# Optimization experiments

Measured on AMD Instinct MI355X. Metric: run time of the kernel, lower is better.

## Reference

```python
import jax, jax.numpy as jnp
import numpy as np

B, SEQ, DIM = 2, 2048, 1024
HEADS, HEAD_DIM = 16, 64
HIDDEN = 2816
EPS = 1e-5
LN_EPS = 1e-5


def rmsnorm(x, w, eps=EPS):
    return x * jax.lax.rsqrt(jnp.mean(x * x, axis=-1, keepdims=True) + eps) * w


def layernorm(x, w, b, eps=LN_EPS):
    mu = jnp.mean(x, axis=-1, keepdims=True)
    var = jnp.mean((x - mu) ** 2, axis=-1, keepdims=True)
    return (x - mu) * jax.lax.rsqrt(var + eps) * w + b


def modulate(x, shift, scale):
    # x: [B,S,D], shift/scale: [B,D]
    return x * (1.0 + scale[:, None, :]) + shift[:, None, :]


def apply_rope(t, cos, sin):
    # t: [B,S,H,D]; cos/sin: [S, D/2] -> complex multiply on (even,odd) pairs
    t = t.reshape(*t.shape[:-1], HEAD_DIM // 2, 2)
    t0, t1 = t[..., 0], t[..., 1]
    c = cos[None, :, None, :]
    s = sin[None, :, None, :]
    o0 = t0 * c - t1 * s
    o1 = t0 * s + t1 * c
    return jnp.stack([o0, o1], axis=-1).reshape(*t.shape[:-2], HEAD_DIM)


def setup_inputs() -> dict:
    key = jax.random.key(0)
    ks = jax.random.split(key, 12)
    def w(k, shape, s=0.02):
        return jax.random.normal(k, shape, dtype=jnp.float32) * s
    x = jax.random.normal(ks[0], (B, SEQ, DIM), dtype=jnp.float32)
    adaln_input = jax.random.normal(ks[1], (B, DIM), dtype=jnp.float32)
    pos = jnp.arange(SEQ, dtype=jnp.float32)
    inv_freq = 1.0 / (10000.0 ** (jnp.arange(0, HEAD_DIM, 2, dtype=jnp.float32) / HEAD_DIM))
    ang = pos[:, None] * inv_freq[None, :]  # [S, D/2]
    return dict(
        x=x, adaln_input=adaln_input,
        freqs_cos=jnp.cos(ang), freqs_sin=jnp.sin(ang),
        wq=w(ks[2], (DIM, DIM)), wk=w(ks[3], (DIM, DIM)),
        wv=w(ks[4], (DIM, DIM)), wo=w(ks[5], (DIM, DIM)),
        q_norm_w=jnp.ones(DIM, jnp.float32), q_norm_b=jnp.zeros(DIM, jnp.float32),
        k_norm_w=jnp.ones(DIM, jnp.float32), k_norm_b=jnp.zeros(DIM, jnp.float32),
        attn_norm_w=jnp.ones(DIM, jnp.float32), ffn_norm_w=jnp.ones(DIM, jnp.float32),
        ada_w=w(ks[6], (DIM, 6 * DIM)), ada_b=jnp.zeros(6 * DIM, jnp.float32),
        w1=w(ks[7], (DIM, HIDDEN)), w2=w(ks[8], (HIDDEN, DIM)), w3=w(ks[9], (DIM, HIDDEN)),
    )


def reference(x, adaln_input, freqs_cos, freqs_sin, wq, wk, wv, wo,
              q_norm_w, q_norm_b, k_norm_w, k_norm_b,
              attn_norm_w, ffn_norm_w, ada_w, ada_b, w1, w2, w3):
    # adaLN modulation: SiLU -> Linear -> 6 chunks of [B, DIM]
    m = jax.nn.silu(adaln_input) @ ada_w + ada_b
    shift_msa, scale_msa, gate_msa, shift_mlp, scale_mlp, gate_mlp = jnp.split(m, 6, axis=1)

    # --- attention branch ---
    h = modulate(rmsnorm(x, attn_norm_w), shift_msa, scale_msa)
    xq = layernorm(h @ wq, q_norm_w, q_norm_b)
    xk = layernorm(h @ wk, k_norm_w, k_norm_b)
    xv = h @ wv
    xq = xq.reshape(B, SEQ, HEADS, HEAD_DIM)
    xk = xk.reshape(B, SEQ, HEADS, HEAD_DIM)
    xv = xv.reshape(B, SEQ, HEADS, HEAD_DIM)
    xq = apply_rope(xq, freqs_cos, freqs_sin)
    xk = apply_rope(xk, freqs_cos, freqs_sin)
    scale = 1.0 / jnp.sqrt(jnp.float32(HEAD_DIM))
    scores = jnp.einsum('bshd,bthd->bhst', xq, xk) * scale  # [B,H,S,S]
    probs = jax.nn.softmax(scores, axis=-1)
    attn = jnp.einsum('bhst,bthd->bshd', probs, xv).reshape(B, SEQ, DIM)
    attn = attn @ wo
    x = x + gate_msa[:, None, :] * attn

    # --- MLP branch (SwiGLU) ---
    h = modulate(rmsnorm(x, ffn_norm_w), shift_mlp, scale_mlp)
    ffn = (jax.nn.silu(h @ w1) * (h @ w3)) @ w2
    x = x + gate_mlp[:, None, :] * ffn
    return x
```

## Files before the change

kernel.cpp:

```cpp
#include <hip/hip_runtime.h>
#include <hip/hip_bf16.h>

#define B_   2
#define S_   2048
#define D_   1024
#define H_   16
#define HD_  64
#define HID_ 2816

typedef unsigned short u16;
typedef unsigned int   u32;
typedef __attribute__((ext_vector_type(8))) short short8;
typedef __attribute__((ext_vector_type(4))) float f32x4;
typedef __attribute__((ext_vector_type(2))) float f32x2;
typedef __attribute__((ext_vector_type(4))) u32   u32x4;
typedef __attribute__((ext_vector_type(2))) unsigned uvec2;

static __device__ __forceinline__ float bf2f(u16 u){ return __uint_as_float(((u32)u)<<16); }
static __device__ __forceinline__ u16 f2bf(float f){
  u32 u = __float_as_uint(f);
  u32 r = (u + 0x7FFFu + ((u>>16)&1u)) >> 16;
  return (u16)r;
}
static __device__ __forceinline__ u16 f2bfr(float f){
  return (u16)((__float_as_uint(f) + 0x8000u) >> 16);
}
static __device__ __forceinline__ u32 cvtpk(float lo, float hi){
  u32 r; asm("v_cvt_pk_bf16_f32 %0, %1, %2" : "=v"(r) : "v"(lo), "v"(hi)); return r;
}
static __device__ __forceinline__ float vmax3(float a, float b, float c){
  float d; asm("v_max3_f32 %0, %1, %2, %3" : "=v"(d) : "v"(a), "v"(b), "v"(c)); return d;
}
static __device__ __forceinline__ f32x2 pkadd(f32x2 a, f32x2 b){
  f32x2 d; asm("v_pk_add_f32 %0, %1, %2" : "=v"(d) : "v"(a), "v"(b)); return d;
}
static __device__ __forceinline__ void plswap16(float x, float& a, float& b){
#if __has_builtin(__builtin_amdgcn_permlane16_swap)
  uvec2 r = __builtin_amdgcn_permlane16_swap(__float_as_uint(x), __float_as_uint(x), false, false);
  a = __uint_as_float(r[0]); b = __uint_as_float(r[1]);
#else
  a = x; b = __shfl_xor(x, 16, 64);
#endif
}
static __device__ __forceinline__ void plswap32(float x, float& a, float& b){
#if __has_builtin(__builtin_amdgcn_permlane32_swap)
  uvec2 r = __builtin_amdgcn_permlane32_swap(__float_as_uint(x), __float_as_uint(x), false, false);
  a = __uint_as_float(r[0]); b = __uint_as_float(r[1]);
#else
  a = x; b = __shfl_xor(x, 32, 64);
#endif
}

static __device__ __forceinline__ void ld4(const u16* p, float* v){
  ushort4 t = *reinterpret_cast<const ushort4*>(p);
  v[0]=bf2f(t.x); v[1]=bf2f(t.y); v[2]=bf2f(t.z); v[3]=bf2f(t.w);
}
static __device__ __forceinline__ void st4(u16* p, const float* v){
  ushort4 t; t.x=f2bf(v[0]); t.y=f2bf(v[1]); t.z=f2bf(v[2]); t.w=f2bf(v[3]);
  *reinterpret_cast<ushort4*>(p)=t;
}

static __device__ __forceinline__ float ld1g(const void* p, size_t i, bool f32){
  return f32 ? ((const float*)p)[i] : bf2f(((const u16*)p)[i]);
}
static __device__ __forceinline__ void ld4g(const void* p, size_t i, float* v, bool f32){
  if(f32){
    float4 t = *reinterpret_cast<const float4*>((const float*)p + i);
    v[0]=t.x; v[1]=t.y; v[2]=t.z; v[3]=t.w;
  }else{
    ushort4 t = *reinterpret_cast<const ushort4*>((const u16*)p + i);
    v[0]=bf2f(t.x); v[1]=bf2f(t.y); v[2]=bf2f(t.z); v[3]=bf2f(t.w);
  }
}

static __device__ __forceinline__ void gl2lds16(const u16* g, const u16* l){
  typedef __attribute__((address_space(3))) u16 lds_u16;
  typedef const __attribute__((address_space(1))) u16 glb_u16;
  __builtin_amdgcn_global_load_lds((glb_u16*)(uintptr_t)g,
                                   (lds_u16*)(u32)(uintptr_t)l, 16, 0, 0);
}

static __device__ __forceinline__ bool is_f32(const u16* fcp){ return fcp[0] == 0; }

static __device__ __forceinline__ float blk_sum(float v, float* red){
  #pragma unroll
  for(int o=32;o;o>>=1) v += __shfl_xor(v,o,64);
  int lane = threadIdx.x & 63, w = threadIdx.x >> 6;
  if(lane==0) red[w]=v;
  __syncthreads();
  float t = red[0]+red[1]+red[2]+red[3];
  __syncthreads();
  return t;
}

__global__ __launch_bounds__(256) void k_wtall(const void* wq, const void* wk, const void* wv,
                                               const void* wo_, const void* w1, const void* w3,
                                               const void* w2_,
                                               u16* qkvT, u16* woT, u16* w13T, u16* w2T,
                                               const u16* fcp, float* m){
  int bid = blockIdx.x;
  if(bid < 48){
    int i = bid*256 + threadIdx.x;
    if(i < 12288) m[i] = 0.f;
    return;
  }
  bid -= 48;
  bool f32 = is_f32(fcp);
  const void* W; u16* dst_base; int Kd, Nd, k0, n0, mode;
  if(bid < 768){
    int z = bid >> 8, rem = bid & 255;
    W = z==0 ? wq : (z==1 ? wk : wv);
    dst_base = qkvT + (size_t)z*1024*1024;
    Kd = 1024; Nd = 1024; k0 = (rem&15)*64; n0 = (rem>>4)*64; mode = 0;
  } else if(bid < 1024){
    int rem = bid - 768;
    W = wo_; dst_base = woT;
    Kd = 1024; Nd = 1024; k0 = (rem&15)*64; n0 = (rem>>4)*64; mode = 0;
  } else if(bid < 2432){
    int z = (bid-1024)/704, rem = (bid-1024) - z*704;
    W = z ? w3 : w1; dst_base = w13T;
    Kd = 1024; Nd = HID_; k0 = (rem&15)*64; n0 = (rem>>4)*64; mode = z ? 2 : 1;
  } else {
    int rem = bid - 2432;
    W = w2_; dst_base = w2T;
    Kd = 2816; Nd = 1024;
    int kb = rem % 44, nb = rem / 44;
    k0 = kb*64; n0 = nb*64; mode = 0;
  }
  __shared__ u16 L[64][72];
  int tid = threadIdx.x;
  int r = tid>>2, c0 = (tid&3)*16;
  if(f32){
    const float* Wf = (const float*)W;
    #pragma unroll
    for(int j=0;j<4;j++){
      float4 t = *reinterpret_cast<const float4*>(&Wf[(size_t)(k0+r)*Nd + n0 + c0 + j*4]);
      L[r][c0+j*4+0]=f2bfr(t.x); L[r][c0+j*4+1]=f2bfr(t.y);
      L[r][c0+j*4+2]=f2bfr(t.z); L[r][c0+j*4+3]=f2bfr(t.w);
    }
  }else{
    const u16* Wh = (const u16*)W;
    *reinterpret_cast<short8*>(&L[r][c0]) =
      *reinterpret_cast<const short8*>(&Wh[(size_t)(k0+r)*Nd + n0 + c0]);
    *reinterpret_cast<short8*>(&L[r][c0+8]) =
      *reinterpret_cast<const short8*>(&Wh[(size_t)(k0+r)*Nd + n0 + c0 + 8]);
  }
  __syncthreads();
  int n = tid>>2, kk0 = (tid&3)*16;
  u16 tmp[16];
  #pragma unroll
  for(int j=0;j<16;j++) tmp[j] = L[kk0+j][n];
  int nglob = n0 + n;
  int rw = (mode==0) ? nglob : ((nglob>>5)<<6) + (nglob&31) + (mode==2 ? 32 : 0);
  u16* dst = dst_base + (size_t)rw*Kd + k0 + kk0;
  *reinterpret_cast<short8*>(dst)   = *reinterpret_cast<const short8*>(tmp);
  *reinterpret_cast<short8*>(dst+8) = *reinterpret_cast<const short8*>(tmp+8);
}

__global__ __launch_bounds__(256) void k_adaln(const void* a, const void* W, const void* bias,
                                               float* m, const u16* fcp){
  bool f32 = is_f32(fcp);
  __shared__ float sl[2][128];
  int bk = blockIdx.y;
  {
    int bb = threadIdx.x >> 7, kk = threadIdx.x & 127;
    float x = ld1g(a, bb*D_ + bk*128 + kk, f32);
    sl[bb][kk] = x/(1.f+__expf(-x));
  }
  __syncthreads();
  int n = blockIdx.x*256 + threadIdx.x;
  float p0 = 0.f, p1 = 0.f;
  for(int kk=0;kk<128;kk++){
    float w = ld1g(W, (size_t)(bk*128+kk)*6144 + n, f32);
    p0 += sl[0][kk]*w; p1 += sl[1][kk]*w;
  }
  if(bk==0){ float bv = ld1g(bias, n, f32); p0 += bv; p1 += bv; }
  atomicAdd(&m[n], p0);
  atomicAdd(&m[6144+n], p1);
}

__global__ __launch_bounds__(256) void k_rms_mod(const void* x, const void* nw, const float* m,
                                                 u16* h, int shift_off, int scale_off,
                                                 const u16* fcp){
  bool f32 = is_f32(fcp);
  __shared__ float red[4];
  int row = blockIdx.x; int b = row >> 11;
  int d0 = threadIdx.x*4;
  float v[4]; ld4g(x, (size_t)row*D_ + d0, v, f32);
  float ss = v[0]*v[0]+v[1]*v[1]+v[2]*v[2]+v[3]*v[3];
  float tot = blk_sum(ss, red);
  float r = rsqrtf(tot*(1.f/D_) + 1e-5f);
  const float* mb = m + b*6144;
  float wn[4]; ld4g(nw, d0, wn, f32);
  float o[4];
  #pragma unroll
  for(int j=0;j<4;j++){
    int d = d0+j;
    o[j] = v[j]*r*wn[j]*(1.f+mb[scale_off+d]) + mb[shift_off+d];
  }
  st4(h + (size_t)row*D_ + d0, o);
}

__global__ __launch_bounds__(256) void k_resid_rms(const void* x, const u16* y, const float* m,
                                                   const void* nw, float* x2, u16* h,
                                                   const u16* fcp){
  bool f32 = is_f32(fcp);
  __shared__ float red[4];
  int row = blockIdx.x; int b = row >> 11;
  int d0 = threadIdx.x*4;
  size_t i4 = (size_t)row*D_ + d0;
  float xv[4], yv[4];
  ld4g(x, i4, xv, f32); ld4(y+i4, yv);
  const float* mb = m + b*6144;
  float v[4];
  #pragma unroll
  for(int j=0;j<4;j++) v[j] = xv[j] + mb[2048+d0+j]*yv[j];
  float4 t; t.x=v[0]; t.y=v[1]; t.z=v[2]; t.w=v[3];
  *reinterpret_cast<float4*>(x2+i4) = t;
  float ss = v[0]*v[0]+v[1]*v[1]+v[2]*v[2]+v[3]*v[3];
  float tot = blk_sum(ss, red);
  float r = rsqrtf(tot*(1.f/D_) + 1e-5f);
  float wn[4]; ld4g(nw, d0, wn, f32);
  float o[4];
  #pragma unroll
  for(int j=0;j<4;j++)
    o[j] = v[j]*r*wn[j]*(1.f+mb[4096+d0+j]) + mb[3072+d0+j];
  st4(h + i4, o);
}

__global__ __launch_bounds__(256) void k_ln_rope2(u16* t, const void* qw, const void* qb,
                                                  const void* kw, const void* kb2,
                                                  const void* fc, const void* fs){
  bool f32 = is_f32((const u16*)fc);
  __shared__ float red[4];
  int row = blockIdx.x; int s = row & (S_-1);
  const void* w  = blockIdx.y ? kw  : qw;
  const void* bb = blockIdx.y ? kb2 : qb;
  int d0 = threadIdx.x*4;
  u16* tp = t + (size_t)row*3072 + blockIdx.y*1024 + d0;
  float v[4]; ld4(tp, v);
  float sm = v[0]+v[1]+v[2]+v[3];
  float sq = v[0]*v[0]+v[1]*v[1]+v[2]*v[2]+v[3]*v[3];
  float tsm = blk_sum(sm, red);
  float tsq = blk_sum(sq, red);
  float mu  = tsm*(1.f/D_);
  float var = tsq*(1.f/D_) - mu*mu;
  float rs  = rsqrtf(var + 1e-5f);
  float wv[4], bv[4]; ld4g(w, d0, wv, f32); ld4g(bb, d0, bv, f32);
  float y[4];
  #pragma unroll
  for(int j=0;j<4;j++) y[j] = (v[j]-mu)*rs*wv[j] + bv[j];
  int pos = d0 & 63; int i0 = pos>>1;
  float c0 = ld1g(fc, s*32+i0,   f32), s0 = ld1g(fs, s*32+i0,   f32);
  float c1 = ld1g(fc, s*32+i0+1, f32), s1 = ld1g(fs, s*32+i0+1, f32);
  float o[4];
  o[0] = y[0]*c0 - y[1]*s0;
  o[1] = y[0]*s0 + y[1]*c0;
  o[2] = y[2]*c1 - y[3]*s1;
  o[3] = y[2]*s1 + y[3]*c1;
  st4(tp, o);
}

template<int TM, int EPI>
__global__ __launch_bounds__(256) void k_gemm_mfma(const u16* A, int lda, const u16* BT, int ldb,
                                                   u16* C, int N, int K,
                                                   const float* x2, const float* mg,
                                                   void* outp, const u16* fcp){
  __shared__ __align__(16) u16 As[2][TM*64];
  __shared__ __align__(16) u16 Bs[2][128*64];
  int tid = threadIdx.x, lane = tid&63, w = tid>>6;
  int col = lane&15, quad = lane>>4;
  int row0 = blockIdx.y*TM, col0 = blockIdx.x*128;
  const u16* Ab = A  + (size_t)row0*lda;
  const u16* Bb = BT + (size_t)col0*ldb;
  constexpr int MI = TM/32;
  int wm = (w>>1)*(TM/2);
  int wn = (w&1)*64;
  f32x4 acc[MI][4];
  #pragma unroll
  for(int i=0;i<MI;i++)
    #pragma unroll
    for(int j=0;j<4;j++) acc[i][j] = (f32x4){0.f,0.f,0.f,0.f};

  const int T = K/64;
  {
    #pragma unroll
    for(int i=0;i<TM/32;i++){
      int c = i*256 + w*64 + lane;
      int r = c>>3, s = c&7, gs = s ^ (r&7);
      gl2lds16(Ab + (size_t)r*lda + gs*8, &As[0][0] + (size_t)c*8);
    }
    #pragma unroll
    for(int i=0;i<4;i++){
      int c = i*256 + w*64 + lane;
      int r = c>>3, s = c&7, gs = s ^ (r&7);
      gl2lds16(Bb + (size_t)r*ldb + gs*8, &Bs[0][0] + (size_t)c*8);
    }
  }
  __syncthreads();

  for(int t=0;t<T;t++){
    if(t+1 < T){
      int k0 = (t+1)*64, b = (t+1)&1;
      #pragma unroll
      for(int i=0;i<TM/32;i++){
        int c = i*256 + w*64 + lane;
        int r = c>>3, s = c&7, gs = s ^ (r&7);
        gl2lds16(Ab + (size_t)r*lda + k0 + gs*8, &As[b][0] + (size_t)c*8);
      }
      #pragma unroll
      for(int i=0;i<4;i++){
        int c = i*256 + w*64 + lane;
        int r = c>>3, s = c&7, gs = s ^ (r&7);
        gl2lds16(Bb + (size_t)r*ldb + k0 + gs*8, &Bs[b][0] + (size_t)c*8);
      }
    }
    const u16* Ac = &As[t&1][0];
    const u16* Bc = &Bs[t&1][0];
    #pragma unroll
    for(int ks=0;ks<64;ks+=32){
      short8 af[MI], bfr[4];
      #pragma unroll
      for(int mi=0;mi<MI;mi++){
        int r = wm+mi*16+col;
        int sch = ((ks>>3) + quad) ^ (col&7);
        af[mi] = *reinterpret_cast<const short8*>(&Ac[r*64 + sch*8]);
      }
      #pragma unroll
      for(int ni=0;ni<4;ni++){
        int r = wn+ni*16+col;
        int sch = ((ks>>3) + quad) ^ (col&7);
        bfr[ni] = *reinterpret_cast<const short8*>(&Bc[r*64 + sch*8]);
      }
      #pragma unroll
      for(int mi=0;mi<MI;mi++)
        #pragma unroll
        for(int ni=0;ni<4;ni++)
          acc[mi][ni] = __builtin_amdgcn_mfma_f32_16x16x32_bf16(af[mi], bfr[ni], acc[mi][ni], 0,0,0);
    }
    __syncthreads();
  }
  if constexpr(EPI==0){
    #pragma unroll
    for(int mi=0;mi<MI;mi++)
      #pragma unroll
      for(int r=0;r<4;r++){
        size_t rowoff = (size_t)(row0+wm+mi*16+quad*4+r)*N + col0 + wn;
        #pragma unroll
        for(int ni=0;ni<4;ni++)
          C[rowoff + ni*16 + col] = f2bfr(acc[mi][ni][r]);
      }
  } else if constexpr(EPI==1){
    int cb = blockIdx.x*64 + (wn?32:0) + col;
    #pragma unroll
    for(int mi=0;mi<MI;mi++)
      #pragma unroll
      for(int r=0;r<4;r++){
        int row = row0+wm+mi*16+quad*4+r;
        u16* gp = C + (size_t)row*HID_ + cb;
        #pragma unroll
        for(int ni=0;ni<2;ni++){
          float a = acc[mi][ni][r], cc = acc[mi][ni+2][r];
          float sv = a * __builtin_amdgcn_rcpf(1.f + __builtin_amdgcn_exp2f(-1.4426950f*a));
          gp[ni*16] = f2bfr(sv*cc);
        }
      }
  } else {
    bool f32o = is_f32(fcp);
    #pragma unroll
    for(int mi=0;mi<MI;mi++)
      #pragma unroll
      for(int r=0;r<4;r++){
        int row = row0+wm+mi*16+quad*4+r;
        int b = row >> 11;
        #pragma unroll
        for(int ni=0;ni<4;ni++){
          int cc = col0 + wn + ni*16 + col;
          float v = x2[(size_t)row*D_ + cc] + mg[b*6144 + 5120 + cc]*acc[mi][ni][r];
          if(f32o) ((float*)outp)[(size_t)row*D_ + cc] = v;
          else     ((u16*)outp)[(size_t)row*D_ + cc]   = f2bfr(v);
        }
      }
  }
}

__global__ __launch_bounds__(256) void k_vt(const u16* v, int vstr, u16* vt){
  __shared__ u16 L[64][72];
  int tid = threadIdx.x;
  int wg = blockIdx.x;
  int kblk = wg & 31; int bh = wg >> 5; int h = bh & 15, b = bh >> 4;
  int row = tid>>2, c0 = (tid&3)*16;
  const u16* src = v + (size_t)(b*S_ + kblk*64 + row)*vstr + h*HD_ + c0;
  *reinterpret_cast<short8*>(&L[row][c0])   = *reinterpret_cast<const short8*>(src);
  *reinterpret_cast<short8*>(&L[row][c0+8]) = *reinterpret_cast<const short8*>(src+8);
  __syncthreads();
  int hd = tid>>2, k0 = (tid&3)*16;
  u16 tmp[16];
  #pragma unroll
  for(int j=0;j<16;j++) tmp[j] = L[k0+j][hd];
  u16* dst = vt + ((size_t)bh*HD_ + hd)*S_ + kblk*64 + k0;
  *reinterpret_cast<short8*>(dst)   = *reinterpret_cast<const short8*>(tmp);
  *reinterpret_cast<short8*>(dst+8) = *reinterpret_cast<const short8*>(tmp+8);
}

__global__ __launch_bounds__(256, 2) void k_attn_mfma(const u16* q, const u16* k, const u16* vt,
                                                      u16* o, int qks){
  __shared__ __align__(16) u16 Ks[2][64*64];
  __shared__ __align__(16) u16 Vs[2][64*64];
  int tid = threadIdx.x, lane = tid & 63, wid = tid >> 6;
  int col = lane & 15, quad = lane >> 4;
  int c7 = col & 7;
  int wg = ((blockIdx.x & 7) << 6) + (blockIdx.x >> 3);
  int qb = wg & 15; int bh = wg >> 4; int h = bh & 15, b = bh >> 4;

  const u16* kb  = k  + (size_t)b*S_*qks + h*HD_;
  const u16* vtb = vt + (size_t)bh*HD_*S_;

  short8 qa[2][2];
  {
    const float qscale = 0.18033688f;
    const u16* qp = q + (size_t)(b*S_ + qb*128 + wid*16 + col)*qks + h*HD_ + quad*8;
    #pragma unroll
    for(int g=0;g<2;g++){
      short8 t0 = *reinterpret_cast<const short8*>(qp + (size_t)g*64*qks);
      short8 t1 = *reinterpret_cast<const short8*>(qp + (size_t)g*64*qks + 32);
      #pragma unroll
      for(int j=0;j<8;j++){
        qa[g][0][j] = (short)f2bf(bf2f((u16)t0[j])*qscale);
        qa[g][1][j] = (short)f2bf(bf2f((u16)t1[j])*qscale);
      }
    }
  }
  short8 vone;
  #pragma unroll
  for(int j=0;j<8;j++) vone[j] = (short)0x3F80;

  float m_i[2] = {-1e30f, -1e30f};
  f32x2 nm[2]; nm[0] = (f32x2){1e30f,1e30f}; nm[1] = (f32x2){1e30f,1e30f};
  f32x4 accl[2];
  accl[0] = (f32x4){0.f,0.f,0.f,0.f}; accl[1] = (f32x4){0.f,0.f,0.f,0.f};
  f32x4 acc[2][4];
  #pragma unroll
  for(int g=0;g<2;g++)
    #pragma unroll
    for(int t=0;t<4;t++) acc[g][t] = (f32x4){0.f,0.f,0.f,0.f};

  int l0 = tid>>3;
  int l1 = 32 + l0;
  int gs = ((tid&7) ^ (l0&7))*8;
  int kl0 = 32*(l0>>5) + 8*((l0>>2)&3) + 4*((l0>>4)&1) + (l0&3);
  int kl1 = 32*(l1>>5) + 8*((l1>>2)&3) + 4*((l1>>4)&1) + (l1&3);
  const u16* kp0 = kb + (size_t)kl0*qks + gs;
  const u16* kp1 = kb + (size_t)kl1*qks + gs;
  const u16* vp0 = vtb + (size_t)l0*S_ + gs;
  const u16* vp1 = vtb + (size_t)l1*S_ + gs;

  gl2lds16(kp0, &Ks[0][tid*8]);
  gl2lds16(kp1, &Ks[0][2048 + tid*8]);
  gl2lds16(vp0, &Vs[0][tid*8]);
  gl2lds16(vp1, &Vs[0][2048 + tid*8]);

  for(int i=0;i<32;i++){
    __syncthreads();
    const u16* Kc = Ks[i&1];
    const u16* Vc = Vs[i&1];
    if(i < 31){
      size_t off = (size_t)(i+1)*64;
      u16* Kn = (u16*)Ks[(i+1)&1];
      u16* Vn = (u16*)Vs[(i+1)&1];
      gl2lds16(kp0 + off*qks, &Kn[tid*8]);
      gl2lds16(kp1 + off*qks, &Kn[2048 + tid*8]);
      gl2lds16(vp0 + off,     &Vn[tid*8]);
      gl2lds16(vp1 + off,     &Vn[2048 + tid*8]);
    }

    f32x4 st[2][4];
    __builtin_amdgcn_s_setprio(1);
    #pragma unroll
    for(int mt=0;mt<4;mt++){
      short8 ka0 = *reinterpret_cast<const short8*>(&Kc[(mt*16+col)*64 + ((quad  ) ^ c7)*8]);
      short8 ka1 = *reinterpret_cast<const short8*>(&Kc[(mt*16+col)*64 + ((quad+4) ^ c7)*8]);
      f32x4 z = (f32x4){0.f,0.f,0.f,0.f};
      st[0][mt] = __builtin_amdgcn_mfma_f32_16x16x32_bf16(ka0, qa[0][0], z, 0,0,0);
      st[1][mt] = __builtin_amdgcn_mfma_f32_16x16x32_bf16(ka0, qa[1][0], z, 0,0,0);
      st[0][mt] = __builtin_amdgcn_mfma_f32_16x16x32_bf16(ka1, qa[0][1], st[0][mt], 0,0,0);
      st[1][mt] = __builtin_amdgcn_mfma_f32_16x16x32_bf16(ka1, qa[1][1], st[1][mt], 0,0,0);
    }
    __builtin_amdgcn_s_setprio(0);

    u32x4 pws[2][2];
    #pragma unroll
    for(int g=0;g<2;g++){
      float t0 = vmax3(st[g][0][0], st[g][0][1], st[g][0][2]);
      float t1 = vmax3(st[g][0][3], st[g][1][0], st[g][1][1]);
      float t2 = vmax3(st[g][1][2], st[g][1][3], st[g][2][0]);
      float t3 = vmax3(st[g][2][1], st[g][2][2], st[g][2][3]);
      float t4 = vmax3(st[g][3][0], st[g][3][1], st[g][3][2]);
      float cm = fmaxf(vmax3(t0, t1, t2), vmax3(t3, t4, st[g][3][3]));
      { float a, bb2; plswap16(cm, a, bb2); cm = fmaxf(a, bb2);
        plswap32(cm, a, bb2); cm = fmaxf(a, bb2); }
      if(__any(cm - m_i[g] > 8.f)){
        float mn = fmaxf(m_i[g], cm);
        float al = __builtin_amdgcn_exp2f(m_i[g] - mn);
        m_i[g] = mn;
        nm[g] = (f32x2){-mn, -mn};
        accl[g][0] *= al;
        #pragma unroll
        for(int t=0;t<4;t++) acc[g][t] *= al;
      }
      float pe[4][4];
      #pragma unroll
      for(int mt=0;mt<4;mt++){
        f32x2 lo = pkadd(st[g][mt].xy, nm[g]);
        f32x2 hi = pkadd(st[g][mt].zw, nm[g]);
        pe[mt][0] = __builtin_amdgcn_exp2f(lo.x);
        pe[mt][1] = __builtin_amdgcn_exp2f(lo.y);
        pe[mt][2] = __builtin_amdgcn_exp2f(hi.x);
        pe[mt][3] = __builtin_amdgcn_exp2f(hi.y);
      }
      #pragma unroll
      for(int w=0;w<2;w++){
        pws[g][w][0] = cvtpk(pe[2*w][0],   pe[2*w][1]);
        pws[g][w][1] = cvtpk(pe[2*w][2],   pe[2*w][3]);
        pws[g][w][2] = cvtpk(pe[2*w+1][0], pe[2*w+1][1]);
        pws[g][w][3] = cvtpk(pe[2*w+1][2], pe[2*w+1][3]);
      }
    }

    __builtin_amdgcn_s_setprio(1);
    #pragma unroll
    for(int w=0;w<2;w++){
      short8 pb0 = *reinterpret_cast<short8*>(&pws[0][w]);
      short8 pb1 = *reinterpret_cast<short8*>(&pws[1][w]);
      #pragma unroll
      for(int ht=0;ht<4;ht++){
        short8 vf = *reinterpret_cast<const short8*>(&Vc[(ht*16+col)*64 + ((w*4+quad) ^ c7)*8]);
        acc[0][ht] = __builtin_amdgcn_mfma_f32_16x16x32_bf16(vf, pb0, acc[0][ht], 0,0,0);
        acc[1][ht] = __builtin_amdgcn_mfma_f32_16x16x32_bf16(vf, pb1, acc[1][ht], 0,0,0);
      }
      accl[0] = __builtin_amdgcn_mfma_f32_16x16x32_bf16(vone, pb0, accl[0], 0,0,0);
      accl[1] = __builtin_amdgcn_mfma_f32_16x16x32_bf16(vone, pb1, accl[1], 0,0,0);
    }
    __builtin_amdgcn_s_setprio(0);
  }
  #pragma unroll
  for(int g=0;g<2;g++){
    float inv = __builtin_amdgcn_rcpf(accl[g][0]);
    u16* ob = o + (size_t)(b*S_ + qb*128 + g*64 + wid*16 + col)*D_ + h*HD_;
    #pragma unroll
    for(int ht=0;ht<4;ht++){
      uint2 t;
      t.x = cvtpk(acc[g][ht][0]*inv, acc[g][ht][1]*inv);
      t.y = cvtpk(acc[g][ht][2]*inv, acc[g][ht][3]*inv);
      *reinterpret_cast<uint2*>(ob + ht*16 + quad*4) = t;
    }
  }
}

extern "C" void kernel_launch(void* const* d_in, const int* in_sizes, int n_in,
                              void* d_out, int out_size, void* d_ws, size_t ws_size,
                              hipStream_t stream){
  const void* x   = d_in[0];
  const void* ada = d_in[1];
  const void* fc  = d_in[2];
  const void* fs  = d_in[3];
  const void* wq  = d_in[4];
  const void* wk  = d_in[5];
  const void* wv  = d_in[6];
  const void* wo  = d_in[7];
  const void* qnw = d_in[8];
  const void* qnb = d_in[9];
  const void* knw = d_in[10];
  const void* knb = d_in[11];
  const void* anw = d_in[12];
  const void* fnw = d_in[13];
  const void* aw  = d_in[14];
  const void* ab  = d_in[15];
  const void* w1  = d_in[16];
  const void* w2  = d_in[17];
  const void* w3  = d_in[18];
  char* ws = (char*)d_ws;
  const size_t MB = 1u<<20;
  const u16* fcp = (const u16*)fc;

  float* m    = (float*)(ws + 4096);
  u16*  hbuf  = (u16*)(ws + 1*MB);
  u16*  xqkv  = (u16*)(ws + 9*MB);
  float* x2   = (float*)(ws + 9*MB);
  u16*  proj  = (u16*)(ws + 25*MB);
  u16*  woT   = (u16*)(ws + 33*MB);
  u16*  w13T  = (u16*)(ws + 35*MB);
  u16*  w2T   = (u16*)(ws + 46*MB);
  u16*  g     = (u16*)(ws + 52*MB);
  u16*  qkvT  = (u16*)(ws + 52*MB);
  u16*  vt    = (u16*)(ws + 58*MB);

  dim3 blk(256);

  k_wtall<<<dim3(3184), blk, 0, stream>>>(wq, wk, wv, wo, w1, w3, w2,
                                          qkvT, woT, w13T, w2T, fcp, m);
  k_adaln<<<dim3(24,8), blk, 0, stream>>>(ada, aw, ab, m, fcp);
  k_rms_mod<<<dim3(B_*S_), blk, 0, stream>>>(x, anw, m, hbuf, 0, 1024, fcp);

  k_gemm_mfma<128,0><<<dim3(24,32), blk, 0, stream>>>(hbuf, 1024, qkvT, 1024, xqkv,
                                                      3072, 1024, nullptr, nullptr, nullptr, fcp);
  k_ln_rope2<<<dim3(B_*S_,2), blk, 0, stream>>>(xqkv, qnw, qnb, knw, knb, fc, fs);
  k_vt<<<dim3(B_*H_*S_/64), blk, 0, stream>>>(xqkv + 2048, 3072, vt);
  k_attn_mfma<<<dim3(B_*H_*S_/128), blk, 0, stream>>>(xqkv, xqkv + 1024, vt, hbuf, 3072);

  k_gemm_mfma<64,0><<<dim3(8,64), blk, 0, stream>>>(hbuf, 1024, woT, 1024, proj,
                                                    1024, 1024, nullptr, nullptr, nullptr, fcp);
  k_resid_rms<<<dim3(B_*S_), blk, 0, stream>>>(x, proj, m, fnw, x2, hbuf, fcp);

  k_gemm_mfma<128,1><<<dim3(44,32), blk, 0, stream>>>(hbuf, 1024, w13T, 1024, g,
                                                      5632, 1024, nullptr, nullptr, nullptr, fcp);
  k_gemm_mfma<64,2><<<dim3(8,64), blk, 0, stream>>>(g, 2816, w2T, 2816, nullptr,
                                                    1024, 2816, x2, m, d_out, fcp);
}
```

Baseline: 389.5 us.

## Fuse LN-RoPE with V transpose and add XCD-aware tile swizzle to GEMMs

Merges the q/k LayerNorm+RoPE kernel and the V transpose kernel into one launch, using the block index to pick the path. Adds an optional block remapping to the GEMM so that consecutive tiles assigned to the same XCD share B columns, which should improve L2 reuse. The remapping is enabled for the QKV and W1/W3 GEMMs. It saves one launch and may improve cache locality, at the cost of index arithmetic and a shared-memory footprint that covers both paths.

```diff
diff --git a/kernel.cpp b/kernel.cpp
--- a/kernel.cpp
+++ b/kernel.cpp
@@ -228,40 +228,61 @@
   st4(h + i4, o);
 }
 
-__global__ __launch_bounds__(256) void k_ln_rope2(u16* t, const void* qw, const void* qb,
-                                                  const void* kw, const void* kb2,
-                                                  const void* fc, const void* fs){
-  bool f32 = is_f32((const u16*)fc);
-  __shared__ float red[4];
-  int row = blockIdx.x; int s = row & (S_-1);
-  const void* w  = blockIdx.y ? kw  : qw;
-  const void* bb = blockIdx.y ? kb2 : qb;
-  int d0 = threadIdx.x*4;
-  u16* tp = t + (size_t)row*3072 + blockIdx.y*1024 + d0;
-  float v[4]; ld4(tp, v);
-  float sm = v[0]+v[1]+v[2]+v[3];
-  float sq = v[0]*v[0]+v[1]*v[1]+v[2]*v[2]+v[3]*v[3];
-  float tsm = blk_sum(sm, red);
-  float tsq = blk_sum(sq, red);
-  float mu  = tsm*(1.f/D_);
-  float var = tsq*(1.f/D_) - mu*mu;
-  float rs  = rsqrtf(var + 1e-5f);
-  float wv[4], bv[4]; ld4g(w, d0, wv, f32); ld4g(bb, d0, bv, f32);
-  float y[4];
-  #pragma unroll
-  for(int j=0;j<4;j++) y[j] = (v[j]-mu)*rs*wv[j] + bv[j];
-  int pos = d0 & 63; int i0 = pos>>1;
-  float c0 = ld1g(fc, s*32+i0,   f32), s0 = ld1g(fs, s*32+i0,   f32);
-  float c1 = ld1g(fc, s*32+i0+1, f32), s1 = ld1g(fs, s*32+i0+1, f32);
-  float o[4];
-  o[0] = y[0]*c0 - y[1]*s0;
-  o[1] = y[0]*s0 + y[1]*c0;
-  o[2] = y[2]*c1 - y[3]*s1;
-  o[3] = y[2]*s1 + y[3]*c1;
-  st4(tp, o);
-}
-
-template<int TM, int EPI>
+__global__ __launch_bounds__(256) void k_lnrope_vt(u16* t, const void* qw, const void* qb,
+                                                   const void* kw, const void* kb2,
+                                                   const void* fc, const void* fs, u16* vt){
+  int bid = blockIdx.x;
+  int tid = threadIdx.x;
+  if(bid < 8192){
+    bool f32 = is_f32((const u16*)fc);
+    __shared__ float red[4];
+    int row = bid >> 1; int s = row & (S_-1);
+    int y2 = bid & 1;
+    const void* w  = y2 ? kw  : qw;
+    const void* bb = y2 ? kb2 : qb;
+    int d0 = tid*4;
+    u16* tp = t + (size_t)row*3072 + y2*1024 + d0;
+    float v[4]; ld4(tp, v);
+    float sm = v[0]+v[1]+v[2]+v[3];
+    float sq = v[0]*v[0]+v[1]*v[1]+v[2]*v[2]+v[3]*v[3];
+    float tsm = blk_sum(sm, red);
+    float tsq = blk_sum(sq, red);
+    float mu  = tsm*(1.f/D_);
+    float var = tsq*(1.f/D_) - mu*mu;
+    float rs  = rsqrtf(var + 1e-5f);
+    float wv[4], bv[4]; ld4g(w, d0, wv, f32); ld4g(bb, d0, bv, f32);
+    float y[4];
+    #pragma unroll
+    for(int j=0;j<4;j++) y[j] = (v[j]-mu)*rs*wv[j] + bv[j];
+    int pos = d0 & 63; int i0 = pos>>1;
+    float c0 = ld1g(fc, s*32+i0,   f32), s0 = ld1g(fs, s*32+i0,   f32);
+    float c1 = ld1g(fc, s*32+i0+1, f32), s1 = ld1g(fs, s*32+i0+1, f32);
+    float o[4];
+    o[0] = y[0]*c0 - y[1]*s0;
+    o[1] = y[0]*s0 + y[1]*c0;
+    o[2] = y[2]*c1 - y[3]*s1;
+    o[3] = y[2]*s1 + y[3]*c1;
+    st4(tp, o);
+  } else {
+    int wg = bid - 8192;
+    __shared__ u16 L[64][72];
+    int kblk = wg & 31; int bh = wg >> 5; int h = bh & 15, b = bh >> 4;
+    int row = tid>>2, c0 = (tid&3)*16;
+    const u16* src = t + (size_t)(b*S_ + kblk*64 + row)*3072 + 2048 + h*HD_ + c0;
+    *reinterpret_cast<short8*>(&L[row][c0])   = *reinterpret_cast<const short8*>(src);
+    *reinterpret_cast<short8*>(&L[row][c0+8]) = *reinterpret_cast<const short8*>(src+8);
+    __syncthreads();
+    int hd = tid>>2, k0 = (tid&3)*16;
+    u16 tmp[16];
+    #pragma unroll
+    for(int j=0;j<16;j++) tmp[j] = L[k0+j][hd];
+    u16* dst = vt + ((size_t)bh*HD_ + hd)*S_ + kblk*64 + k0;
+    *reinterpret_cast<short8*>(dst)   = *reinterpret_cast<const short8*>(tmp);
+    *reinterpret_cast<short8*>(dst+8) = *reinterpret_cast<const short8*>(tmp+8);
+  }
+}
+
+template<int TM, int EPI, int SWZ>
 __global__ __launch_bounds__(256) void k_gemm_mfma(const u16* A, int lda, const u16* BT, int ldb,
                                                    u16* C, int N, int K,
                                                    const float* x2, const float* mg,
@@ -270,7 +291,17 @@
   __shared__ __align__(16) u16 Bs[2][128*64];
   int tid = threadIdx.x, lane = tid&63, w = tid>>6;
   int col = lane&15, quad = lane>>4;
-  int row0 = blockIdx.y*TM, col0 = blockIdx.x*128;
+  int bx, by;
+  if constexpr(SWZ){
+    int gx = gridDim.x, gy = gridDim.y;
+    int nwg = gx*gy;
+    int bid = blockIdx.y*gx + blockIdx.x;
+    int xcd = bid & 7, pos = bid >> 3;
+    int q8 = nwg >> 3, r8 = nwg & 7;
+    int lin = (xcd < r8 ? xcd*(q8+1) : r8*(q8+1) + (xcd-r8)*q8) + pos;
+    bx = lin / gy; by = lin - bx*gy;
+  } else { bx = blockIdx.x; by = blockIdx.y; }
+  int row0 = by*TM, col0 = bx*128;
   const u16* Ab = A  + (size_t)row0*lda;
   const u16* Bb = BT + (size_t)col0*ldb;
   constexpr int MI = TM/32;
@@ -351,7 +382,7 @@
           C[rowoff + ni*16 + col] = f2bfr(acc[mi][ni][r]);
       }
   } else if constexpr(EPI==1){
-    int cb = blockIdx.x*64 + (wn?32:0) + col;
+    int cb = (col0>>1) + (wn?32:0) + col;
     #pragma unroll
     for(int mi=0;mi<MI;mi++)
       #pragma unroll
@@ -382,25 +413,6 @@
         }
       }
   }
-}
-
-__global__ __launch_bounds__(256) void k_vt(const u16* v, int vstr, u16* vt){
-  __shared__ u16 L[64][72];
-  int tid = threadIdx.x;
-  int wg = blockIdx.x;
-  int kblk = wg & 31; int bh = wg >> 5; int h = bh & 15, b = bh >> 4;
-  int row = tid>>2, c0 = (tid&3)*16;
-  const u16* src = v + (size_t)(b*S_ + kblk*64 + row)*vstr + h*HD_ + c0;
-  *reinterpret_cast<short8*>(&L[row][c0])   = *reinterpret_cast<const short8*>(src);
-  *reinterpret_cast<short8*>(&L[row][c0+8]) = *reinterpret_cast<const short8*>(src+8);
-  __syncthreads();
-  int hd = tid>>2, k0 = (tid&3)*16;
-  u16 tmp[16];
-  #pragma unroll
-  for(int j=0;j<16;j++) tmp[j] = L[k0+j][hd];
-  u16* dst = vt + ((size_t)bh*HD_ + hd)*S_ + kblk*64 + k0;
-  *reinterpret_cast<short8*>(dst)   = *reinterpret_cast<const short8*>(tmp);
-  *reinterpret_cast<short8*>(dst+8) = *reinterpret_cast<const short8*>(tmp+8);
 }
 
 __global__ __launch_bounds__(256, 2) void k_attn_mfma(const u16* q, const u16* k, const u16* vt,
@@ -602,18 +614,17 @@
   k_adaln<<<dim3(24,8), blk, 0, stream>>>(ada, aw, ab, m, fcp);
   k_rms_mod<<<dim3(B_*S_), blk, 0, stream>>>(x, anw, m, hbuf, 0, 1024, fcp);
 
-  k_gemm_mfma<128,0><<<dim3(24,32), blk, 0, stream>>>(hbuf, 1024, qkvT, 1024, xqkv,
-                                                      3072, 1024, nullptr, nullptr, nullptr, fcp);
-  k_ln_rope2<<<dim3(B_*S_,2), blk, 0, stream>>>(xqkv, qnw, qnb, knw, knb, fc, fs);
-  k_vt<<<dim3(B_*H_*S_/64), blk, 0, stream>>>(xqkv + 2048, 3072, vt);
+  k_gemm_mfma<128,0,1><<<dim3(24,32), blk, 0, stream>>>(hbuf, 1024, qkvT, 1024, xqkv,
+                                                        3072, 1024, nullptr, nullptr, nullptr, fcp);
+  k_lnrope_vt<<<dim3(9216), blk, 0, stream>>>(xqkv, qnw, qnb, knw, knb, fc, fs, vt);
   k_attn_mfma<<<dim3(B_*H_*S_/128), blk, 0, stream>>>(xqkv, xqkv + 1024, vt, hbuf, 3072);
 
-  k_gemm_mfma<64,0><<<dim3(8,64), blk, 0, stream>>>(hbuf, 1024, woT, 1024, proj,
-                                                    1024, 1024, nullptr, nullptr, nullptr, fcp);
+  k_gemm_mfma<64,0,0><<<dim3(8,64), blk, 0, stream>>>(hbuf, 1024, woT, 1024, proj,
+                                                      1024, 1024, nullptr, nullptr, nullptr, fcp);
   k_resid_rms<<<dim3(B_*S_), blk, 0, stream>>>(x, proj, m, fnw, x2, hbuf, fcp);
 
-  k_gemm_mfma<128,1><<<dim3(44,32), blk, 0, stream>>>(hbuf, 1024, w13T, 1024, g,
-                                                      5632, 1024, nullptr, nullptr, nullptr, fcp);
-  k_gemm_mfma<64,2><<<dim3(8,64), blk, 0, stream>>>(g, 2816, w2T, 2816, nullptr,
-                                                    1024, 2816, x2, m, d_out, fcp);
-}
+  k_gemm_mfma<128,1,1><<<dim3(44,32), blk, 0, stream>>>(hbuf, 1024, w13T, 1024, g,
+                                                        5632, 1024, nullptr, nullptr, nullptr, fcp);
+  k_gemm_mfma<64,2,0><<<dim3(8,64), blk, 0, stream>>>(g, 2816, w2T, 2816, nullptr,
+                                                      1024, 2816, x2, m, d_out, fcp);
+}
```

Result: slower. 397.3 us (+2.0%).
